# Kernel tuning notes

Hardware: AMD Instinct MI355X
Metric: run time of the kernel (lower is better)

Reference implementation:

```python
import jax, jax.numpy as jnp
import numpy as np

B, D_IN, D_OUT, L = 4096, 1024, 1024, 32

def setup_inputs() -> dict:
    key = jax.random.key(0)
    k1, k2, k3 = jax.random.split(key, 3)
    x = jax.random.normal(k1, (B, D_IN), dtype=jnp.float32)
    # xavier_normal for gw: std = sqrt(2/(fan_in+fan_out))
    gw = jax.random.normal(k2, (D_IN, L), dtype=jnp.float32) * np.sqrt(2.0 / (D_IN + L))
    gb = jnp.zeros((L,), dtype=jnp.float32)
    # kaiming_normal (linear): std = sqrt(1/fan_in); stored as [out, in, leafs]
    pw = jax.random.normal(k3, (D_OUT, D_IN, L), dtype=jnp.float32) * np.sqrt(1.0 / D_IN)
    pb = jnp.zeros((D_OUT, L), dtype=jnp.float32)
    return {"x": x, "gw": gw, "gb": gb, "pw": pw, "pb": pb}

def reference(x, gw, gb, pw, pb):
    # gatings: [B, L], softmax over leafs (dropout p=0 -> identity)
    gatings = jax.nn.softmax(x @ gw + gb, axis=1)
    # Original math: result[b,o] = sum_i (sum_l pw[o,i,l] * g[b,l]) * x[b,i] + sum_l pb[o,l] * g[b,l]
    # Equivalent reordering: project x per leaf, then combine with gates.
    proj = jnp.einsum('bi,oil->bol', x, pw)          # [B, D_OUT, L]
    result = jnp.einsum('bol,bl->bo', proj, gatings) + gatings @ pb.T
    return result
```

## Files before the change

### kernel.cpp

```cpp
#include <hip/hip_runtime.h>
#include <stdint.h>

#define NB   4096
#define DIN  1024
#define DOUT 1024
#define NL   32
#define KPW  (DIN * NL)
#define KTOT (KPW + 64)
#define BKT  64
#define KITERS (KTOT / BKT)
#define NSPLIT 4

typedef __attribute__((ext_vector_type(8))) short short8;
typedef __attribute__((ext_vector_type(8))) unsigned short ushort8;
typedef __attribute__((ext_vector_type(4))) float floatx4;

__device__ __forceinline__ unsigned short f2bf(float v) {
    uint32_t u = __float_as_uint(v);
    return (unsigned short)((u + 0x7FFFu + ((u >> 16) & 1u)) >> 16);
}

__device__ __forceinline__ uint32_t f2bf2(float a, float b) {
    uint32_t ua = __float_as_uint(a), ub = __float_as_uint(b);
    ua += 0x7FFFu + ((ua >> 16) & 1u);
    ub += 0x7FFFu + ((ub >> 16) & 1u);
    return __builtin_amdgcn_perm(ub, ua, 0x07060302u);
}

__device__ __forceinline__ void async_ld16(const void* g, void* l) {
    __builtin_amdgcn_global_load_lds(
        (const __attribute__((address_space(1))) void*)g,
        (__attribute__((address_space(3))) void*)l, 16, 0, 0);
}

__global__ __launch_bounds__(256) void prep_fused(
    const float* __restrict__ x, const float* __restrict__ gw,
    const float* __restrict__ gb, const float* __restrict__ pw,
    const float* __restrict__ pb, float* __restrict__ g,
    unsigned short* __restrict__ pwb, float* __restrict__ C)
{
    const int id = blockIdx.x;
    const int t  = threadIdx.x;

    if (id < DOUT) {
        const int o = id;
        const float* src = pw + (size_t)o * KPW;
        unsigned short* dst = pwb + (size_t)o * KTOT;
        #pragma unroll 2
        for (int s = 0; s < 16; ++s) {
            const int k = (s * 256 + t) * 8;
            const float4 a = *(const float4*)(src + k);
            const float4 c = *(const float4*)(src + k + 4);
            ushort8 o8;
            o8[0] = f2bf(a.x); o8[1] = f2bf(a.y); o8[2] = f2bf(a.z); o8[3] = f2bf(a.w);
            o8[4] = f2bf(c.x); o8[5] = f2bf(c.y); o8[6] = f2bf(c.z); o8[7] = f2bf(c.w);
            *(ushort8*)(dst + k) = o8;
        }
        if (t < 8) {
            ushort8 o8;
            #pragma unroll
            for (int j = 0; j < 8; ++j) {
                const int l = t * 8 + j;
                o8[j] = (l < NL) ? f2bf(pb[(size_t)o * NL + l]) : (unsigned short)0;
            }
            *(ushort8*)(dst + KPW + t * 8) = o8;
        }
    } else if (id < DOUT + NB / 4) {
        const int wave = t >> 6;
        const int lane = t & 63;
        const int b = (id - DOUT) * 4 + wave;
        const int l = lane & 31;
        const int c = lane >> 5;
        const float* xrow = x + (size_t)b * DIN;
        float p0 = 0.f, p1 = 0.f, p2 = 0.f, p3 = 0.f;
        const int i0 = c * 512;
        #pragma unroll 2
        for (int j = 0; j < 512; j += 4) {
            const int i = i0 + j;
            p0 = fmaf(xrow[i + 0], gw[(i + 0) * NL + l], p0);
            p1 = fmaf(xrow[i + 1], gw[(i + 1) * NL + l], p1);
            p2 = fmaf(xrow[i + 2], gw[(i + 2) * NL + l], p2);
            p3 = fmaf(xrow[i + 3], gw[(i + 3) * NL + l], p3);
        }
        float p = (p0 + p1) + (p2 + p3);
        p += __shfl_xor(p, 32);
        const float logit = p + gb[l];
        float m = logit;
        for (int off = 16; off > 0; off >>= 1) m = fmaxf(m, __shfl_xor(m, off));
        const float e = __expf(logit - m);
        float s = e;
        for (int off = 16; off > 0; off >>= 1) s += __shfl_xor(s, off);
        if (lane < NL) g[(size_t)b * NL + l] = e / s;
    } else {
        const int zb = id - (DOUT + NB / 4);
        float4* dst = (float4*)C + (size_t)zb * (256 * 64) + t;
        const float4 z4 = {0.f, 0.f, 0.f, 0.f};
        #pragma unroll 4
        for (int s = 0; s < 64; ++s) dst[s * 256] = z4;
    }
}

__global__ __launch_bounds__(256, 4) void gemm_splitk(
    const float* __restrict__ X,
    const float* __restrict__ G,
    const unsigned short* __restrict__ Bw,
    float* __restrict__ C)
{
    __shared__ unsigned short As[128 * BKT];
    __shared__ unsigned short Bs[128 * BKT];

    const int t    = threadIdx.x;
    const int wave = t >> 6;
    const int lane = t & 63;

    const int id  = blockIdx.x;
    const int xcd = id & 7;
    const int s_  = id >> 3;
    const int bn  = (s_ & 7) * 128;
    const int idx = xcd * 16 + (s_ >> 3);
    const int bm  = (idx & 31) * 128;
    const int z   = idx >> 5;
    const int it0 = z * 128 + (z ? 1 : 0);
    const int it1 = (z + 1) * 128 + 1;

    const int wm = (wave >> 1) * 64;
    const int wn = (wave & 1) * 64;
    const int ml   = lane & 15;
    const int quad = lane >> 4;
    const int xorm = ml & 7;

    const int row0 = t >> 3;
    const int uc   = (((t & 7) ^ ((t >> 3) & 7)) * 8);
    const unsigned short* Bg = Bw + (size_t)(bn + row0) * KTOT + uc + (size_t)it0 * BKT;
    unsigned short* Bl = Bs + wave * 512;

    const int r   = t >> 1;
    const int lh  = (t & 1) * 16;
    const int rx  = r & 7;
    const float* xp = X + (size_t)(bm + r) * DIN;
    unsigned short* Aw = As + r * BKT;
    float gq[16];
    {
        const float* gp = G + (size_t)(bm + r) * NL + lh;
        #pragma unroll
        for (int q = 0; q < 4; ++q) {
            const float4 v = *(const float4*)(gp + q * 4);
            gq[q * 4 + 0] = v.x; gq[q * 4 + 1] = v.y;
            gq[q * 4 + 2] = v.z; gq[q * 4 + 3] = v.w;
        }
    }

    floatx4 acc[4][4] = {};
    float2 xv = *(const float2*)(xp + min(it0 * 2, DIN - 2));

    for (int it = it0; it < it1; ++it) {
        #pragma unroll
        for (int s = 0; s < 4; ++s)
            async_ld16(Bg + (size_t)(s * 32) * KTOT, Bl + s * 2048);
        Bg += BKT;

        const bool inb = (it * 2) < DIN;
        const float xa = inb ? xv.x : 1.0f;
        const float xb = inb ? xv.y : 0.0f;
        xv = *(const float2*)(xp + min((it + 1) * 2, DIN - 2));

        #pragma unroll
        for (int ii = 0; ii < 2; ++ii) {
            const float xs = ii ? xb : xa;
            #pragma unroll
            for (int j = 0; j < 2; ++j) {
                uint4 v;
                v.x = f2bf2(xs * gq[j * 8 + 0], xs * gq[j * 8 + 1]);
                v.y = f2bf2(xs * gq[j * 8 + 2], xs * gq[j * 8 + 3]);
                v.z = f2bf2(xs * gq[j * 8 + 4], xs * gq[j * 8 + 5]);
                v.w = f2bf2(xs * gq[j * 8 + 6], xs * gq[j * 8 + 7]);
                const int c = ii * 4 + (t & 1) * 2 + j;
                *(uint4*)(Aw + ((c ^ rx) * 8)) = v;
            }
        }
        __syncthreads();

        #pragma unroll
        for (int kk = 0; kk < 2; ++kk) {
            const int swz = ((kk * 4 + quad) ^ xorm) * 8;
            short8 af[4], bf[4];
            #pragma unroll
            for (int im = 0; im < 4; ++im)
                af[im] = *(const short8*)(As + (wm + im * 16 + ml) * BKT + swz);
            #pragma unroll
            for (int in = 0; in < 4; ++in)
                bf[in] = *(const short8*)(Bs + (wn + in * 16 + ml) * BKT + swz);
            #pragma unroll
            for (int im = 0; im < 4; ++im)
                #pragma unroll
                for (int in = 0; in < 4; ++in)
                    acc[im][in] = __builtin_amdgcn_mfma_f32_16x16x32_bf16(
                        af[im], bf[in], acc[im][in], 0, 0, 0);
        }
        __syncthreads();
    }

    #pragma unroll
    for (int im = 0; im < 4; ++im)
        #pragma unroll
        for (int in = 0; in < 4; ++in) {
            const int row = bm + wm + im * 16 + quad * 4;
            const int col = bn + wn + in * 16 + ml;
            #pragma unroll
            for (int rr = 0; rr < 4; ++rr)
                atomicAdd(&C[(size_t)(row + rr) * DOUT + col], acc[im][in][rr]);
        }
}

extern "C" void kernel_launch(void* const* d_in, const int* in_sizes, int n_in,
                              void* d_out, int out_size, void* d_ws, size_t ws_size,
                              hipStream_t stream) {
    const float* x  = (const float*)d_in[0];
    const float* gw = (const float*)d_in[1];
    const float* gb = (const float*)d_in[2];
    const float* pw = (const float*)d_in[3];
    const float* pb = (const float*)d_in[4];
    float* out = (float*)d_out;

    float* g            = (float*)d_ws;
    unsigned short* pwb = (unsigned short*)((char*)d_ws + (1 << 20));

    prep_fused<<<DOUT + NB / 4 + 64, 256, 0, stream>>>(x, gw, gb, pw, pb, g, pwb, out);
    gemm_splitk<<<(DOUT / 128) * (NB / 128) * NSPLIT, 256, 0, stream>>>(x, g, pwb, out);
}
```

Measured before the change: 357.5 us.

## Rewrite split-K GEMM as 256x256 tile with triple-buffered 8-phase pipeline

Result: slower. 445.6 us (+24.6%).

```diff
diff --git a/kernel.cpp b/kernel.cpp
--- a/kernel.cpp
+++ b/kernel.cpp
@@ -8,7 +8,6 @@
 #define KPW  (DIN * NL)
 #define KTOT (KPW + 64)
 #define BKT  64
-#define KITERS (KTOT / BKT)
 #define NSPLIT 4
 
 typedef __attribute__((ext_vector_type(8))) short short8;
@@ -100,112 +99,199 @@
     }
 }
 
-__global__ __launch_bounds__(256, 4) void gemm_splitk(
+__global__ __launch_bounds__(512, 2) void gemm_8phase(
     const float* __restrict__ X,
     const float* __restrict__ G,
     const unsigned short* __restrict__ Bw,
     float* __restrict__ C)
 {
-    __shared__ unsigned short As[128 * BKT];
-    __shared__ unsigned short Bs[128 * BKT];
+    __shared__ __align__(16) unsigned short Ash[256 * BKT];
+    __shared__ __align__(16) unsigned short Bsh[3][256 * BKT];
 
     const int t    = threadIdx.x;
     const int wave = t >> 6;
     const int lane = t & 63;
 
-    const int id  = blockIdx.x;
-    const int xcd = id & 7;
-    const int s_  = id >> 3;
-    const int bn  = (s_ & 7) * 128;
-    const int idx = xcd * 16 + (s_ >> 3);
-    const int bm  = (idx & 31) * 128;
-    const int z   = idx >> 5;
-    const int it0 = z * 128 + (z ? 1 : 0);
-    const int it1 = (z + 1) * 128 + 1;
-
-    const int wm = (wave >> 1) * 64;
-    const int wn = (wave & 1) * 64;
+    const int bid   = blockIdx.x;
+    const int xcd   = bid & 7;
+    const int seq   = bid >> 3;
+    const int combo = xcd + 8 * (seq >> 4);
+    const int bm    = (seq & 15) * 256;
+    const int bn    = (combo & 3) * 256;
+    const int z     = combo >> 2;
+    const int it0   = z * 128 + (z ? 1 : 0);
+    const int it1   = (z + 1) * 128 + 1;
+
+    const int wr   = wave >> 2;
+    const int wc   = wave & 3;
     const int ml   = lane & 15;
     const int quad = lane >> 4;
-    const int xorm = ml & 7;
-
-    const int row0 = t >> 3;
-    const int uc   = (((t & 7) ^ ((t >> 3) & 7)) * 8);
-    const unsigned short* Bg = Bw + (size_t)(bn + row0) * KTOT + uc + (size_t)it0 * BKT;
-    unsigned short* Bl = Bs + wave * 512;
-
-    const int r   = t >> 1;
-    const int lh  = (t & 1) * 16;
-    const int rx  = r & 7;
+    const int xm   = ml & 7;
+    const int sw0  = (quad ^ xm) * 8;
+    const int sw1  = ((4 + quad) ^ xm) * 8;
+
+    const int trow = t >> 3;
+    const unsigned short* Bg = Bw + (size_t)(bn + trow) * KTOT
+                             + (((t & 7) ^ (trow & 7)) * 8);
+    const int lbase = wave * 512;
+
+    const int r = t >> 1, rx = r & 7, lsel = (t & 1) * 2;
     const float* xp = X + (size_t)(bm + r) * DIN;
-    unsigned short* Aw = As + r * BKT;
+    unsigned short* Aw = Ash + r * BKT;
+
     float gq[16];
     {
-        const float* gp = G + (size_t)(bm + r) * NL + lh;
+        const float* gp = G + (size_t)(bm + r) * NL + (t & 1) * 16;
         #pragma unroll
         for (int q = 0; q < 4; ++q) {
             const float4 v = *(const float4*)(gp + q * 4);
-            gq[q * 4 + 0] = v.x; gq[q * 4 + 1] = v.y;
-            gq[q * 4 + 2] = v.z; gq[q * 4 + 3] = v.w;
+            gq[q*4+0] = v.x; gq[q*4+1] = v.y; gq[q*4+2] = v.z; gq[q*4+3] = v.w;
         }
     }
 
-    floatx4 acc[4][4] = {};
-    float2 xv = *(const float2*)(xp + min(it0 * 2, DIN - 2));
-
-    for (int it = it0; it < it1; ++it) {
-        #pragma unroll
-        for (int s = 0; s < 4; ++s)
-            async_ld16(Bg + (size_t)(s * 32) * KTOT, Bl + s * 2048);
-        Bg += BKT;
-
-        const bool inb = (it * 2) < DIN;
+    const unsigned short* aB = Ash + (wr * 128 + ml) * BKT;
+
+    floatx4 acc[8][4] = {};
+    short8 af[8], bf[4];
+    float2 xv;
+
+    auto buildA = [&](int T) {
+        const bool inb = (T * 2) < DIN;
         const float xa = inb ? xv.x : 1.0f;
         const float xb = inb ? xv.y : 0.0f;
-        xv = *(const float2*)(xp + min((it + 1) * 2, DIN - 2));
-
         #pragma unroll
         for (int ii = 0; ii < 2; ++ii) {
             const float xs = ii ? xb : xa;
             #pragma unroll
             for (int j = 0; j < 2; ++j) {
                 uint4 v;
-                v.x = f2bf2(xs * gq[j * 8 + 0], xs * gq[j * 8 + 1]);
-                v.y = f2bf2(xs * gq[j * 8 + 2], xs * gq[j * 8 + 3]);
-                v.z = f2bf2(xs * gq[j * 8 + 4], xs * gq[j * 8 + 5]);
-                v.w = f2bf2(xs * gq[j * 8 + 6], xs * gq[j * 8 + 7]);
-                const int c = ii * 4 + (t & 1) * 2 + j;
+                v.x = f2bf2(xs * gq[j*8+0], xs * gq[j*8+1]);
+                v.y = f2bf2(xs * gq[j*8+2], xs * gq[j*8+3]);
+                v.z = f2bf2(xs * gq[j*8+4], xs * gq[j*8+5]);
+                v.w = f2bf2(xs * gq[j*8+6], xs * gq[j*8+7]);
+                const int c = ii * 4 + lsel + j;
                 *(uint4*)(Aw + ((c ^ rx) * 8)) = v;
             }
         }
-        __syncthreads();
-
-        #pragma unroll
-        for (int kk = 0; kk < 2; ++kk) {
-            const int swz = ((kk * 4 + quad) ^ xorm) * 8;
-            short8 af[4], bf[4];
-            #pragma unroll
-            for (int im = 0; im < 4; ++im)
-                af[im] = *(const short8*)(As + (wm + im * 16 + ml) * BKT + swz);
-            #pragma unroll
-            for (int in = 0; in < 4; ++in)
-                bf[in] = *(const short8*)(Bs + (wn + in * 16 + ml) * BKT + swz);
-            #pragma unroll
-            for (int im = 0; im < 4; ++im)
+    };
+
+    xv = *(const float2*)(xp + it0 * 2);
+    {
+        const unsigned short* s0 = Bg + (size_t)it0 * BKT;
+        #pragma unroll
+        for (int s = 0; s < 4; ++s)
+            async_ld16(s0 + (size_t)s * 64 * KTOT, &Bsh[0][lbase + s * 4096]);
+        const unsigned short* s1 = s0 + BKT;
+        #pragma unroll
+        for (int s = 0; s < 4; ++s)
+            async_ld16(s1 + (size_t)s * 64 * KTOT, &Bsh[1][lbase + s * 4096]);
+    }
+    buildA(it0);
+    asm volatile("s_waitcnt vmcnt(4) lgkmcnt(0)" ::: "memory");
+    __builtin_amdgcn_s_barrier();
+
+    int pr = 0, ps = 2;
+    for (int it = it0; it < it1; ++it) {
+        const unsigned short* bB = Bsh[pr] + (wc * 64 + ml) * BKT;
+        const int tf = (it + 2 < it1) ? (it + 2) : (it1 - 1);
+        const unsigned short* sf = Bg + (size_t)tf * BKT;
+        unsigned short* db = &Bsh[ps][lbase];
+
+        async_ld16(sf,                     db);
+        async_ld16(sf + (size_t)64 * KTOT, db + 4096);
+        xv = *(const float2*)(xp + (((it + 1) * 2 < DIN) ? (it + 1) * 2 : (DIN - 2)));
+        #pragma unroll
+        for (int im = 0; im < 4; ++im) {
+            af[im*2+0] = *(const short8*)(aB + (im*16)*BKT + sw0);
+            af[im*2+1] = *(const short8*)(aB + (im*16)*BKT + sw1);
+        }
+        #pragma unroll
+        for (int in = 0; in < 2; ++in) {
+            bf[in*2+0] = *(const short8*)(bB + (in*16)*BKT + sw0);
+            bf[in*2+1] = *(const short8*)(bB + (in*16)*BKT + sw1);
+        }
+        __builtin_amdgcn_s_barrier();
+        __builtin_amdgcn_s_setprio(1);
+        #pragma unroll
+        for (int im = 0; im < 4; ++im)
+            #pragma unroll
+            for (int in = 0; in < 2; ++in)
                 #pragma unroll
-                for (int in = 0; in < 4; ++in)
+                for (int kk = 0; kk < 2; ++kk)
                     acc[im][in] = __builtin_amdgcn_mfma_f32_16x16x32_bf16(
-                        af[im], bf[in], acc[im][in], 0, 0, 0);
-        }
-        __syncthreads();
+                        af[im*2+kk], bf[in*2+kk], acc[im][in], 0, 0, 0);
+        __builtin_amdgcn_s_setprio(0);
+        __builtin_amdgcn_s_barrier();
+
+        async_ld16(sf + (size_t)128 * KTOT, db + 2 * 4096);
+        async_ld16(sf + (size_t)192 * KTOT, db + 3 * 4096);
+        #pragma unroll
+        for (int in = 0; in < 2; ++in) {
+            bf[in*2+0] = *(const short8*)(bB + ((in+2)*16)*BKT + sw0);
+            bf[in*2+1] = *(const short8*)(bB + ((in+2)*16)*BKT + sw1);
+        }
+        __builtin_amdgcn_s_barrier();
+        __builtin_amdgcn_s_setprio(1);
+        #pragma unroll
+        for (int im = 0; im < 4; ++im)
+            #pragma unroll
+            for (int in = 0; in < 2; ++in)
+                #pragma unroll
+                for (int kk = 0; kk < 2; ++kk)
+                    acc[im][in+2] = __builtin_amdgcn_mfma_f32_16x16x32_bf16(
+                        af[im*2+kk], bf[in*2+kk], acc[im][in+2], 0, 0, 0);
+        __builtin_amdgcn_s_setprio(0);
+        __builtin_amdgcn_s_barrier();
+
+        #pragma unroll
+        for (int im = 0; im < 4; ++im) {
+            af[im*2+0] = *(const short8*)(aB + ((im+4)*16)*BKT + sw0);
+            af[im*2+1] = *(const short8*)(aB + ((im+4)*16)*BKT + sw1);
+        }
+        __builtin_amdgcn_s_barrier();
+        __builtin_amdgcn_s_setprio(1);
+        #pragma unroll
+        for (int im = 0; im < 4; ++im)
+            #pragma unroll
+            for (int in = 0; in < 2; ++in)
+                #pragma unroll
+                for (int kk = 0; kk < 2; ++kk)
+                    acc[im+4][in+2] = __builtin_amdgcn_mfma_f32_16x16x32_bf16(
+                        af[im*2+kk], bf[in*2+kk], acc[im+4][in+2], 0, 0, 0);
+        __builtin_amdgcn_s_setprio(0);
+        __builtin_amdgcn_s_barrier();
+
+        #pragma unroll
+        for (int in = 0; in < 2; ++in) {
+            bf[in*2+0] = *(const short8*)(bB + (in*16)*BKT + sw0);
+            bf[in*2+1] = *(const short8*)(bB + (in*16)*BKT + sw1);
+        }
+        if (it + 1 < it1) buildA(it + 1);
+        asm volatile("s_waitcnt vmcnt(2)" ::: "memory");
+        __builtin_amdgcn_s_barrier();
+        __builtin_amdgcn_s_setprio(1);
+        #pragma unroll
+        for (int im = 0; im < 4; ++im)
+            #pragma unroll
+            for (int in = 0; in < 2; ++in)
+                #pragma unroll
+                for (int kk = 0; kk < 2; ++kk)
+                    acc[im+4][in] = __builtin_amdgcn_mfma_f32_16x16x32_bf16(
+                        af[im*2+kk], bf[in*2+kk], acc[im+4][in], 0, 0, 0);
+        __builtin_amdgcn_s_setprio(0);
+        asm volatile("s_waitcnt lgkmcnt(0)" ::: "memory");
+        __builtin_amdgcn_s_barrier();
+
+        pr = (pr == 2) ? 0 : pr + 1;
+        ps = (ps == 2) ? 0 : ps + 1;
     }
 
     #pragma unroll
-    for (int im = 0; im < 4; ++im)
+    for (int im = 0; im < 8; ++im)
         #pragma unroll
         for (int in = 0; in < 4; ++in) {
-            const int row = bm + wm + im * 16 + quad * 4;
-            const int col = bn + wn + in * 16 + ml;
+            const int row = bm + wr * 128 + im * 16 + quad * 4;
+            const int col = bn + wc * 64 + in * 16 + ml;
             #pragma unroll
             for (int rr = 0; rr < 4; ++rr)
                 atomicAdd(&C[(size_t)(row + rr) * DOUT + col], acc[im][in][rr]);
@@ -226,5 +312,5 @@
     unsigned short* pwb = (unsigned short*)((char*)d_ws + (1 << 20));
 
     prep_fused<<<DOUT + NB / 4 + 64, 256, 0, stream>>>(x, gw, gb, pw, pb, g, pwb, out);
-    gemm_splitk<<<(DOUT / 128) * (NB / 128) * NSPLIT, 256, 0, stream>>>(x, g, pwb, out);
-}
+    gemm_8phase<<<(DOUT / 256) * (NB / 256) * NSPLIT, 512, 0, stream>>>(x, g, pwb, out);
+}
```

## Double-buffer B tile in LDS with async prefetch of next k-slice

Applied to the files above, without the earlier changes.

New measurement: 457.4 us. 27.9% more time.

```diff
diff --git a/kernel.cpp b/kernel.cpp
--- a/kernel.cpp
+++ b/kernel.cpp
@@ -106,8 +106,8 @@
     const unsigned short* __restrict__ Bw,
     float* __restrict__ C)
 {
-    __shared__ unsigned short As[128 * BKT];
-    __shared__ unsigned short Bs[128 * BKT];
+    __shared__ __align__(16) unsigned short As[128 * BKT];
+    __shared__ __align__(16) unsigned short Bs[2][128 * BKT];
 
     const int t    = threadIdx.x;
     const int wave = t >> 6;
@@ -123,16 +123,16 @@
     const int it0 = z * 128 + (z ? 1 : 0);
     const int it1 = (z + 1) * 128 + 1;
 
-    const int wm = (wave >> 1) * 64;
-    const int wn = (wave & 1) * 64;
+    const int wm   = (wave >> 1) * 64;
+    const int wn   = (wave & 1) * 64;
     const int ml   = lane & 15;
     const int quad = lane >> 4;
     const int xorm = ml & 7;
 
     const int row0 = t >> 3;
     const int uc   = (((t & 7) ^ ((t >> 3) & 7)) * 8);
-    const unsigned short* Bg = Bw + (size_t)(bn + row0) * KTOT + uc + (size_t)it0 * BKT;
-    unsigned short* Bl = Bs + wave * 512;
+    const unsigned short* Bg = Bw + (size_t)(bn + row0) * KTOT + uc;
+    const int lofs = wave * 512;
 
     const int r   = t >> 1;
     const int lh  = (t & 1) * 16;
@@ -151,19 +151,30 @@
     }
 
     floatx4 acc[4][4] = {};
-    float2 xv = *(const float2*)(xp + min(it0 * 2, DIN - 2));
-
+
+    float2 xv_cur = *(const float2*)(xp + min(it0 * 2, DIN - 2));
+    {
+        const unsigned short* s0 = Bg + (size_t)it0 * BKT;
+        #pragma unroll
+        for (int s = 0; s < 4; ++s)
+            async_ld16(s0 + (size_t)(s * 32) * KTOT, &Bs[0][lofs + s * 2048]);
+    }
+    float2 xv_next = *(const float2*)(xp + min((it0 + 1) * 2, DIN - 2));
+
+    int cur = 0;
     for (int it = it0; it < it1; ++it) {
-        #pragma unroll
-        for (int s = 0; s < 4; ++s)
-            async_ld16(Bg + (size_t)(s * 32) * KTOT, Bl + s * 2048);
-        Bg += BKT;
+        {
+            const int tf = (it + 1 < it1) ? (it + 1) : (it1 - 1);
+            const unsigned short* sf = Bg + (size_t)tf * BKT;
+            #pragma unroll
+            for (int s = 0; s < 4; ++s)
+                async_ld16(sf + (size_t)(s * 32) * KTOT,
+                           &Bs[cur ^ 1][lofs + s * 2048]);
+        }
 
         const bool inb = (it * 2) < DIN;
-        const float xa = inb ? xv.x : 1.0f;
-        const float xb = inb ? xv.y : 0.0f;
-        xv = *(const float2*)(xp + min((it + 1) * 2, DIN - 2));
-
+        const float xa = inb ? xv_cur.x : 1.0f;
+        const float xb = inb ? xv_cur.y : 0.0f;
         #pragma unroll
         for (int ii = 0; ii < 2; ++ii) {
             const float xs = ii ? xb : xa;
@@ -178,26 +189,34 @@
                 *(uint4*)(Aw + ((c ^ rx) * 8)) = v;
             }
         }
-        __syncthreads();
+
+        xv_cur  = xv_next;
+        xv_next = *(const float2*)(xp + min((it + 2) * 2, DIN - 2));
+
+        asm volatile("s_waitcnt vmcnt(5) lgkmcnt(0)" ::: "memory");
+        __builtin_amdgcn_s_barrier();
+        __builtin_amdgcn_sched_barrier(0);
 
         #pragma unroll
         for (int kk = 0; kk < 2; ++kk) {
             const int swz = ((kk * 4 + quad) ^ xorm) * 8;
-            short8 af[4], bf[4];
+            short8 af[4], bfr[4];
             #pragma unroll
             for (int im = 0; im < 4; ++im)
                 af[im] = *(const short8*)(As + (wm + im * 16 + ml) * BKT + swz);
             #pragma unroll
             for (int in = 0; in < 4; ++in)
-                bf[in] = *(const short8*)(Bs + (wn + in * 16 + ml) * BKT + swz);
+                bfr[in] = *(const short8*)(&Bs[cur][(wn + in * 16 + ml) * BKT + swz]);
             #pragma unroll
             for (int im = 0; im < 4; ++im)
                 #pragma unroll
                 for (int in = 0; in < 4; ++in)
                     acc[im][in] = __builtin_amdgcn_mfma_f32_16x16x32_bf16(
-                        af[im], bf[in], acc[im][in], 0, 0, 0);
-        }
-        __syncthreads();
+                        af[im], bfr[in], acc[im][in], 0, 0, 0);
+        }
+        __builtin_amdgcn_sched_barrier(0);
+        __builtin_amdgcn_s_barrier();
+        cur ^= 1;
     }
 
     #pragma unroll
```

## Materialize gated bf16 activations and use double-buffered 256x256 split-K GEMM

Applied to the files above, without the earlier changes.

Result: slower. 515.3 us (+44.2%).

```diff
diff --git a/kernel.cpp b/kernel.cpp
--- a/kernel.cpp
+++ b/kernel.cpp
@@ -8,7 +8,6 @@
 #define KPW  (DIN * NL)
 #define KTOT (KPW + 64)
 #define BKT  64
-#define KITERS (KTOT / BKT)
 #define NSPLIT 4
 
 typedef __attribute__((ext_vector_type(8))) short short8;
@@ -31,6 +30,267 @@
     __builtin_amdgcn_global_load_lds(
         (const __attribute__((address_space(1))) void*)g,
         (__attribute__((address_space(3))) void*)l, 16, 0, 0);
+}
+
+
+__global__ __launch_bounds__(256) void prep_y(
+    const float* __restrict__ x, const float* __restrict__ gw,
+    const float* __restrict__ gb, const float* __restrict__ pw,
+    const float* __restrict__ pb, unsigned short* __restrict__ y,
+    unsigned short* __restrict__ pwb, float* __restrict__ C)
+{
+    const int id = blockIdx.x;
+    const int t  = threadIdx.x;
+
+    if (id < DOUT) {
+        const int o = id;
+        const float* src = pw + (size_t)o * KPW;
+        unsigned short* dst = pwb + (size_t)o * KTOT;
+        #pragma unroll 2
+        for (int s = 0; s < 16; ++s) {
+            const int k = (s * 256 + t) * 8;
+            const float4 a = *(const float4*)(src + k);
+            const float4 c = *(const float4*)(src + k + 4);
+            ushort8 o8;
+            o8[0] = f2bf(a.x); o8[1] = f2bf(a.y); o8[2] = f2bf(a.z); o8[3] = f2bf(a.w);
+            o8[4] = f2bf(c.x); o8[5] = f2bf(c.y); o8[6] = f2bf(c.z); o8[7] = f2bf(c.w);
+            *(ushort8*)(dst + k) = o8;
+        }
+        if (t < 8) {
+            ushort8 o8;
+            #pragma unroll
+            for (int j = 0; j < 8; ++j) {
+                const int l = t * 8 + j;
+                o8[j] = (l < NL) ? f2bf(pb[(size_t)o * NL + l]) : (unsigned short)0;
+            }
+            *(ushort8*)(dst + KPW + t * 8) = o8;
+        }
+    } else if (id < DOUT + NB / 4) {
+        __shared__ float gsh[4][NL];
+        const int wave = t >> 6;
+        const int lane = t & 63;
+        const int b0 = (id - DOUT) * 4;
+        {
+            const int b = b0 + wave;
+            const int l = lane & 31;
+            const int c = lane >> 5;
+            const float* xrow = x + (size_t)b * DIN;
+            float p0 = 0.f, p1 = 0.f, p2 = 0.f, p3 = 0.f;
+            const int i0 = c * 512;
+            #pragma unroll 2
+            for (int j = 0; j < 512; j += 4) {
+                const int i = i0 + j;
+                p0 = fmaf(xrow[i + 0], gw[(i + 0) * NL + l], p0);
+                p1 = fmaf(xrow[i + 1], gw[(i + 1) * NL + l], p1);
+                p2 = fmaf(xrow[i + 2], gw[(i + 2) * NL + l], p2);
+                p3 = fmaf(xrow[i + 3], gw[(i + 3) * NL + l], p3);
+            }
+            float p = (p0 + p1) + (p2 + p3);
+            p += __shfl_xor(p, 32);
+            const float logit = p + gb[l];
+            float m = logit;
+            for (int off = 16; off > 0; off >>= 1) m = fmaxf(m, __shfl_xor(m, off));
+            const float e = __expf(logit - m);
+            float s = e;
+            for (int off = 16; off > 0; off >>= 1) s += __shfl_xor(s, off);
+            if (lane < NL) gsh[wave][l] = e / s;
+        }
+        __syncthreads();
+        #pragma unroll 1
+        for (int rr = 0; rr < 4; ++rr) {
+            const int b = b0 + rr;
+            const float* xrow = x + (size_t)b * DIN;
+            unsigned short* yrow = y + (size_t)b * KTOT;
+            float gv[NL];
+            #pragma unroll
+            for (int l = 0; l < NL; ++l) gv[l] = gsh[rr][l];
+            for (int i = t; i < KTOT / 32; i += 256) {
+                const float xv = (i < DIN) ? xrow[i] : (i == DIN ? 1.0f : 0.0f);
+                #pragma unroll
+                for (int cq = 0; cq < 4; ++cq) {
+                    ushort8 o8;
+                    #pragma unroll
+                    for (int jj = 0; jj < 8; ++jj)
+                        o8[jj] = f2bf(xv * gv[cq * 8 + jj]);
+                    *(ushort8*)(yrow + (size_t)i * 32 + cq * 8) = o8;
+                }
+            }
+        }
+    } else {
+        const int zb = id - (DOUT + NB / 4);
+        float4* dst = (float4*)C + (size_t)zb * (256 * 64) + t;
+        const float4 z4 = {0.f, 0.f, 0.f, 0.f};
+        #pragma unroll 4
+        for (int s = 0; s < 64; ++s) dst[s * 256] = z4;
+    }
+}
+
+__global__ __launch_bounds__(512, 2) void gemm_2buf(
+    const unsigned short* __restrict__ Ay,
+    const unsigned short* __restrict__ Bw,
+    float* __restrict__ C)
+{
+    __shared__ __align__(16) unsigned short Ash[2][16384];
+    __shared__ __align__(16) unsigned short Bsh[2][16384];
+
+    const int t    = threadIdx.x;
+    const int wave = t >> 6;
+    const int lane = t & 63;
+
+    const int bid = blockIdx.x;
+    const int xcd = bid & 7;
+    const int loc = bid >> 3;
+    const int q   = xcd * 8 + (loc >> 2);
+    const int bn  = (loc & 3) * 256;
+    const int bm  = (q & 15) * 256;
+    const int z   = q >> 4;
+    const int it0 = z * 128 + (z ? 1 : 0);
+    const int nt  = z ? 128 : 129;
+
+    const int wr   = wave >> 2;
+    const int wc   = wave & 3;
+    const int ml   = lane & 15;
+    const int quad = lane >> 4;
+    const int xm   = ml & 7;
+    const int sw0  = (quad ^ xm) * 8;
+    const int sw1  = ((4 + quad) ^ xm) * 8;
+
+    const int slot = t >> 3;
+    const int sw   = ((t & 7) ^ (slot & 7)) * 8;
+    const unsigned short* a0 = Ay + (size_t)(bm +       slot) * KTOT + sw;
+    const unsigned short* a1 = Ay + (size_t)(bm + 128 + slot) * KTOT + sw;
+    const unsigned short* a2 = Ay + (size_t)(bm +  64 + slot) * KTOT + sw;
+    const unsigned short* a3 = Ay + (size_t)(bm + 192 + slot) * KTOT + sw;
+    const int brow = (slot >> 5) * 64 + (slot & 31);
+    const unsigned short* b0 = Bw + (size_t)(bn +       brow) * KTOT + sw;
+    const unsigned short* b1 = Bw + (size_t)(bn + 128 + brow) * KTOT + sw;
+    const unsigned short* b2 = Bw + (size_t)(bn +  32 + brow) * KTOT + sw;
+    const unsigned short* b3 = Bw + (size_t)(bn + 160 + brow) * KTOT + sw;
+    const int ldst = wave * 512;
+
+    const int ai = (wr * 64 + ml) * 64;
+    const int bi = (wc * 32 + ml) * 64;
+
+    floatx4 acc[8][4] = {};
+    short8 af[8], bfa[4], bfb[4];
+
+    {
+        const size_t ko = (size_t)it0 * BKT;
+        async_ld16(a0 + ko, &Ash[0][ldst]);
+        async_ld16(a1 + ko, &Ash[0][ldst +  4096]);
+        async_ld16(b0 + ko, &Bsh[0][ldst]);
+        async_ld16(b1 + ko, &Bsh[0][ldst +  4096]);
+        async_ld16(a2 + ko, &Ash[0][ldst +  8192]);
+        async_ld16(a3 + ko, &Ash[0][ldst + 12288]);
+        async_ld16(b2 + ko, &Bsh[0][ldst +  8192]);
+        async_ld16(b3 + ko, &Bsh[0][ldst + 12288]);
+    }
+    asm volatile("s_waitcnt vmcnt(0)" ::: "memory");
+    __builtin_amdgcn_s_barrier();
+
+    for (int j = 0; j < nt; ++j) {
+        const int rb = j & 1, sb = rb ^ 1;
+        const unsigned short* aR = &Ash[rb][0];
+        const unsigned short* bR = &Bsh[rb][0];
+        const size_t ko = (size_t)(it0 + ((j + 1 < nt) ? (j + 1) : (nt - 1))) * BKT;
+
+        async_ld16(a0 + ko, &Ash[sb][ldst]);
+        async_ld16(a1 + ko, &Ash[sb][ldst + 4096]);
+        #pragma unroll
+        for (int im = 0; im < 4; ++im) {
+            af[im*2+0] = *(const short8*)(aR + ai + im*1024 + sw0);
+            af[im*2+1] = *(const short8*)(aR + ai + im*1024 + sw1);
+        }
+        #pragma unroll
+        for (int in = 0; in < 2; ++in) {
+            bfa[in*2+0] = *(const short8*)(bR + bi + in*1024 + sw0);
+            bfa[in*2+1] = *(const short8*)(bR + bi + in*1024 + sw1);
+        }
+        asm volatile("s_waitcnt vmcnt(2)" ::: "memory");
+        __builtin_amdgcn_s_barrier();
+        __builtin_amdgcn_s_setprio(1);
+        #pragma unroll
+        for (int im = 0; im < 4; ++im)
+            #pragma unroll
+            for (int in = 0; in < 2; ++in) {
+                acc[im][in] = __builtin_amdgcn_mfma_f32_16x16x32_bf16(
+                    af[im*2+0], bfa[in*2+0], acc[im][in], 0, 0, 0);
+                acc[im][in] = __builtin_amdgcn_mfma_f32_16x16x32_bf16(
+                    af[im*2+1], bfa[in*2+1], acc[im][in], 0, 0, 0);
+            }
+        __builtin_amdgcn_s_setprio(0);
+        __builtin_amdgcn_s_barrier();
+
+        async_ld16(b0 + ko, &Bsh[sb][ldst]);
+        async_ld16(b1 + ko, &Bsh[sb][ldst + 4096]);
+        #pragma unroll
+        for (int in = 0; in < 2; ++in) {
+            bfb[in*2+0] = *(const short8*)(bR + 8192 + bi + in*1024 + sw0);
+            bfb[in*2+1] = *(const short8*)(bR + 8192 + bi + in*1024 + sw1);
+        }
+        __builtin_amdgcn_s_barrier();
+        __builtin_amdgcn_s_setprio(1);
+        #pragma unroll
+        for (int im = 0; im < 4; ++im)
+            #pragma unroll
+            for (int in = 0; in < 2; ++in) {
+                acc[im][in+2] = __builtin_amdgcn_mfma_f32_16x16x32_bf16(
+                    af[im*2+0], bfb[in*2+0], acc[im][in+2], 0, 0, 0);
+                acc[im][in+2] = __builtin_amdgcn_mfma_f32_16x16x32_bf16(
+                    af[im*2+1], bfb[in*2+1], acc[im][in+2], 0, 0, 0);
+            }
+        __builtin_amdgcn_s_setprio(0);
+        __builtin_amdgcn_s_barrier();
+
+        async_ld16(a2 + ko, &Ash[sb][ldst +  8192]);
+        async_ld16(a3 + ko, &Ash[sb][ldst + 12288]);
+        #pragma unroll
+        for (int im = 0; im < 4; ++im) {
+            af[im*2+0] = *(const short8*)(aR + 8192 + ai + im*1024 + sw0);
+            af[im*2+1] = *(const short8*)(aR + 8192 + ai + im*1024 + sw1);
+        }
+        __builtin_amdgcn_s_barrier();
+        __builtin_amdgcn_s_setprio(1);
+        #pragma unroll
+        for (int im = 0; im < 4; ++im)
+            #pragma unroll
+            for (int in = 0; in < 2; ++in) {
+                acc[im+4][in+2] = __builtin_amdgcn_mfma_f32_16x16x32_bf16(
+                    af[im*2+0], bfb[in*2+0], acc[im+4][in+2], 0, 0, 0);
+                acc[im+4][in+2] = __builtin_amdgcn_mfma_f32_16x16x32_bf16(
+                    af[im*2+1], bfb[in*2+1], acc[im+4][in+2], 0, 0, 0);
+            }
+        __builtin_amdgcn_s_setprio(0);
+        __builtin_amdgcn_s_barrier();
+
+        async_ld16(b2 + ko, &Bsh[sb][ldst +  8192]);
+        async_ld16(b3 + ko, &Bsh[sb][ldst + 12288]);
+        asm volatile("s_waitcnt vmcnt(4)" ::: "memory");
+        __builtin_amdgcn_s_barrier();
+        __builtin_amdgcn_s_setprio(1);
+        #pragma unroll
+        for (int im = 0; im < 4; ++im)
+            #pragma unroll
+            for (int in = 0; in < 2; ++in) {
+                acc[im+4][in] = __builtin_amdgcn_mfma_f32_16x16x32_bf16(
+                    af[im*2+0], bfa[in*2+0], acc[im+4][in], 0, 0, 0);
+                acc[im+4][in] = __builtin_amdgcn_mfma_f32_16x16x32_bf16(
+                    af[im*2+1], bfa[in*2+1], acc[im+4][in], 0, 0, 0);
+            }
+        __builtin_amdgcn_s_setprio(0);
+        __builtin_amdgcn_s_barrier();
+    }
+
+    #pragma unroll
+    for (int im = 0; im < 8; ++im)
+        #pragma unroll
+        for (int in = 0; in < 4; ++in) {
+            const int row = bm + wr * 128 + im * 16 + quad * 4;
+            const int col = bn + wc * 64 + in * 16 + ml;
+            #pragma unroll
+            for (int rr = 0; rr < 4; ++rr)
+                atomicAdd(&C[(size_t)(row + rr) * DOUT + col], acc[im][in][rr]);
+        }
 }
 
 __global__ __launch_bounds__(256) void prep_fused(
@@ -101,10 +361,8 @@
 }
 
 __global__ __launch_bounds__(256, 4) void gemm_splitk(
-    const float* __restrict__ X,
-    const float* __restrict__ G,
-    const unsigned short* __restrict__ Bw,
-    float* __restrict__ C)
+    const float* __restrict__ X, const float* __restrict__ G,
+    const unsigned short* __restrict__ Bw, float* __restrict__ C)
 {
     __shared__ unsigned short As[128 * BKT];
     __shared__ unsigned short Bs[128 * BKT];
@@ -123,8 +381,8 @@
     const int it0 = z * 128 + (z ? 1 : 0);
     const int it1 = (z + 1) * 128 + 1;
 
-    const int wm = (wave >> 1) * 64;
-    const int wn = (wave & 1) * 64;
+    const int wm   = (wave >> 1) * 64;
+    const int wn   = (wave & 1) * 64;
     const int ml   = lane & 15;
     const int quad = lane >> 4;
     const int xorm = ml & 7;
@@ -143,10 +401,10 @@
     {
         const float* gp = G + (size_t)(bm + r) * NL + lh;
         #pragma unroll
-        for (int q = 0; q < 4; ++q) {
-            const float4 v = *(const float4*)(gp + q * 4);
-            gq[q * 4 + 0] = v.x; gq[q * 4 + 1] = v.y;
-            gq[q * 4 + 2] = v.z; gq[q * 4 + 3] = v.w;
+        for (int qq = 0; qq < 4; ++qq) {
+            const float4 v = *(const float4*)(gp + qq * 4);
+            gq[qq * 4 + 0] = v.x; gq[qq * 4 + 1] = v.y;
+            gq[qq * 4 + 2] = v.z; gq[qq * 4 + 3] = v.w;
         }
     }
 
@@ -168,13 +426,13 @@
         for (int ii = 0; ii < 2; ++ii) {
             const float xs = ii ? xb : xa;
             #pragma unroll
-            for (int j = 0; j < 2; ++j) {
+            for (int jj = 0; jj < 2; ++jj) {
                 uint4 v;
-                v.x = f2bf2(xs * gq[j * 8 + 0], xs * gq[j * 8 + 1]);
-                v.y = f2bf2(xs * gq[j * 8 + 2], xs * gq[j * 8 + 3]);
-                v.z = f2bf2(xs * gq[j * 8 + 4], xs * gq[j * 8 + 5]);
-                v.w = f2bf2(xs * gq[j * 8 + 6], xs * gq[j * 8 + 7]);
-                const int c = ii * 4 + (t & 1) * 2 + j;
+                v.x = f2bf2(xs * gq[jj * 8 + 0], xs * gq[jj * 8 + 1]);
+                v.y = f2bf2(xs * gq[jj * 8 + 2], xs * gq[jj * 8 + 3]);
+                v.z = f2bf2(xs * gq[jj * 8 + 4], xs * gq[jj * 8 + 5]);
+                v.w = f2bf2(xs * gq[jj * 8 + 6], xs * gq[jj * 8 + 7]);
+                const int c = ii * 4 + (t & 1) * 2 + jj;
                 *(uint4*)(Aw + ((c ^ rx) * 8)) = v;
             }
         }
@@ -183,19 +441,19 @@
         #pragma unroll
         for (int kk = 0; kk < 2; ++kk) {
             const int swz = ((kk * 4 + quad) ^ xorm) * 8;
-            short8 af[4], bf[4];
+            short8 afr[4], bfr[4];
             #pragma unroll
             for (int im = 0; im < 4; ++im)
-                af[im] = *(const short8*)(As + (wm + im * 16 + ml) * BKT + swz);
+                afr[im] = *(const short8*)(As + (wm + im * 16 + ml) * BKT + swz);
             #pragma unroll
             for (int in = 0; in < 4; ++in)
-                bf[in] = *(const short8*)(Bs + (wn + in * 16 + ml) * BKT + swz);
+                bfr[in] = *(const short8*)(Bs + (wn + in * 16 + ml) * BKT + swz);
             #pragma unroll
             for (int im = 0; im < 4; ++im)
                 #pragma unroll
                 for (int in = 0; in < 4; ++in)
                     acc[im][in] = __builtin_amdgcn_mfma_f32_16x16x32_bf16(
-                        af[im], bf[in], acc[im][in], 0, 0, 0);
+                        afr[im], bfr[in], acc[im][in], 0, 0, 0);
         }
         __syncthreads();
     }
@@ -222,9 +480,18 @@
     const float* pb = (const float*)d_in[4];
     float* out = (float*)d_out;
 
-    float* g            = (float*)d_ws;
-    unsigned short* pwb = (unsigned short*)((char*)d_ws + (1 << 20));
-
-    prep_fused<<<DOUT + NB / 4 + 64, 256, 0, stream>>>(x, gw, gb, pw, pb, g, pwb, out);
-    gemm_splitk<<<(DOUT / 128) * (NB / 128) * NSPLIT, 256, 0, stream>>>(x, g, pwb, out);
-}
+    const size_t pwb_bytes = (size_t)DOUT * KTOT * 2;
+    const size_t y_bytes   = (size_t)NB   * KTOT * 2;
+
+    if (ws_size >= pwb_bytes + y_bytes) {
+        unsigned short* pwb = (unsigned short*)d_ws;
+        unsigned short* y   = (unsigned short*)((char*)d_ws + pwb_bytes);
+        prep_y<<<DOUT + NB / 4 + 64, 256, 0, stream>>>(x, gw, gb, pw, pb, y, pwb, out);
+        gemm_2buf<<<256, 512, 0, stream>>>(y, pwb, out);
+    } else {
+        float* g            = (float*)d_ws;
+        unsigned short* pwb = (unsigned short*)((char*)d_ws + (1 << 20));
+        prep_fused<<<DOUT + NB / 4 + 64, 256, 0, stream>>>(x, gw, gb, pw, pb, g, pwb, out);
+        gemm_splitk<<<(DOUT / 128) * (NB / 128) * NSPLIT, 256, 0, stream>>>(x, g, pwb, out);
+    }
+}
```
